# Kernel tuning notes

Measured on AMD Instinct MI355X. Metric: run time of the kernel, lower is better.

## Reference

```python
import jax, jax.numpy as jnp
import numpy as np

H = 16          # num_attention_heads
D = 1024        # hidden_size
HD = D // H     # attention_head_size = 64


def setup_inputs() -> dict:
    key = jax.random.key(0)
    ks = jax.random.split(key, 9)
    s = 1.0 / np.sqrt(D)
    return {
        "hidden_states": jax.random.normal(ks[0], (4, 1024, D), jnp.float32),
        "encoder_hidden_states": jax.random.normal(ks[1], (4, 1024, D), jnp.float32),
        "attention_mask": jnp.zeros((4, 1, 1, 2048), jnp.float32),
        "Wq": jax.random.normal(ks[2], (D, D), jnp.float32) * s,
        "bq": jnp.zeros((D,), jnp.float32),
        "Wk": jax.random.normal(ks[3], (D, D), jnp.float32) * s,
        "bk": jnp.zeros((D,), jnp.float32),
        "Wv": jax.random.normal(ks[4], (D, D), jnp.float32) * s,
        "bv": jnp.zeros((D,), jnp.float32),
    }


def _split_heads(x):
    # [B, S, D] -> [B, H, S, HD]
    B, S, _ = x.shape
    return x.reshape(B, S, H, HD).transpose(0, 2, 1, 3)


def reference(hidden_states, encoder_hidden_states, attention_mask, Wq, bq, Wk, bk, Wv, bv):
    # KV over concat(encoder, decoder); Q over decoder hidden states only.
    all_hidden = jnp.concatenate([encoder_hidden_states, hidden_states], axis=1)  # [B, Skv, D]
    q = _split_heads(hidden_states @ Wq + bq)        # [B, H, Sq, HD]
    k = _split_heads(all_hidden @ Wk + bk)           # [B, H, Skv, HD]
    v = _split_heads(all_hidden @ Wv + bv)           # [B, H, Skv, HD]

    scores = jnp.einsum("bhqd,bhkd->bhqk", q, k) / np.sqrt(HD).astype(np.float32)
    scores = scores + attention_mask                 # additive mask, broadcast
    probs = jax.nn.softmax(scores, axis=-1)          # dropout p=0 (eval)
    ctx = jnp.einsum("bhqk,bhkd->bhqd", probs, v)    # [B, H, Sq, HD]
    B, _, Sq, _ = ctx.shape
    return ctx.transpose(0, 2, 1, 3).reshape(B, Sq, D)
```

## Files before the change

### kernel.cpp

```cpp
#include <hip/hip_runtime.h>


typedef _Float16 f16;
typedef __attribute__((ext_vector_type(4))) _Float16 half4;
typedef __attribute__((ext_vector_type(8))) _Float16 half8;
typedef __attribute__((ext_vector_type(4))) float floatx4;
typedef __attribute__((ext_vector_type(16))) float floatx16;
typedef __attribute__((ext_vector_type(4))) unsigned int uint4v;

#define GLOAD16(gp, lp)                                                        \
    __builtin_amdgcn_global_load_lds(                                          \
        (const __attribute__((address_space(1))) void*)(gp),                   \
        (__attribute__((address_space(3))) void*)(lp), 16, 0, 0)

__global__ void wt_kernel(const float* __restrict__ Wq, const float* __restrict__ Wk,
                          const float* __restrict__ Wv, f16* __restrict__ Wtq,
                          f16* __restrict__ Wtk, f16* __restrict__ Wtv) {
    __shared__ float tile[32][33];
    const float* W = (blockIdx.z == 0) ? Wq : (blockIdx.z == 1) ? Wk : Wv;
    f16* Wt = (blockIdx.z == 0) ? Wtq : (blockIdx.z == 1) ? Wtk : Wtv;
    int k0 = blockIdx.y * 32, n0 = blockIdx.x * 32;
    int tx = threadIdx.x, ty = threadIdx.y;
    #pragma unroll
    for (int i = 0; i < 32; i += 8)
        tile[ty + i][tx] = W[(k0 + ty + i) * 1024 + n0 + tx];
    __syncthreads();
    #pragma unroll
    for (int i = 0; i < 32; i += 8)
        Wt[(n0 + ty + i) * 1024 + k0 + tx] = (f16)tile[tx][ty + i];
}

__global__ void cvt_kernel(const float* __restrict__ hid, const float* __restrict__ enc,
                           f16* __restrict__ Aall) {
    int t = blockIdx.x * 256 + threadIdx.x;
    int rowg = t >> 7, col = (t & 127) * 8;
    int b = rowg >> 11, r = rowg & 2047;
    const float* src = (r < 1024 ? enc + ((size_t)b * 1024 + r) * 1024
                                 : hid + ((size_t)b * 1024 + (r - 1024)) * 1024) + col;
    float4 v0 = *(const float4*)src, v1 = *(const float4*)(src + 4);
    half8 o;
    o[0] = (f16)v0.x; o[1] = (f16)v0.y; o[2] = (f16)v0.z; o[3] = (f16)v0.w;
    o[4] = (f16)v1.x; o[5] = (f16)v1.y; o[6] = (f16)v1.z; o[7] = (f16)v1.w;
    *(half8*)(Aall + (size_t)rowg * 1024 + col) = o;
}

__launch_bounds__(256)
__global__ void qkv_gemm(const f16* __restrict__ Aall,
                         const f16* __restrict__ Wtq, const f16* __restrict__ Wtk,
                         const f16* __restrict__ Wtv,
                         const float* __restrict__ bq, const float* __restrict__ bk,
                         const float* __restrict__ bv,
                         f16* __restrict__ Qw, f16* __restrict__ Kw, f16* __restrict__ Vtw) {
    int mode = blockIdx.z;
    if (mode == 0 && blockIdx.x >= 32) return;
    __shared__ f16 As[2][128 * 32];
    __shared__ f16 Bs[2][128 * 32];

    const f16* Wt = (mode == 0) ? Wtq : (mode == 1) ? Wtk : Wtv;
    const float* bias = (mode == 0) ? bq : (mode == 1) ? bk : bv;
    f16* out = (mode == 0) ? Qw : (mode == 1) ? Kw : Vtw;

    int tid = threadIdx.x;
    int m0 = blockIdx.x * 128, n0 = blockIdx.y * 128;
    int wid = tid >> 6, lane = tid & 63;
    int wm = (wid >> 1) * 64, wn = (wid & 1) * 64;
    int lr = lane & 15, lg = lane >> 4;

    floatx4 acc[4][4];
    #pragma unroll
    for (int i = 0; i < 4; i++)
        #pragma unroll
        for (int j = 0; j < 4; j++) acc[i][j] = (floatx4)(0.f);

    int trow = tid >> 2, tcol = (tid & 3) * 8;
    const f16 *a0g, *a1g;
    {
        int mA0 = m0 + trow, mA1 = mA0 + 64;
        if (mode == 0) {
            int b0 = mA0 >> 10, b1 = mA1 >> 10;
            a0g = Aall + ((size_t)(b0 * 2048 + 1024 + (mA0 & 1023))) * 1024 + tcol;
            a1g = Aall + ((size_t)(b1 * 2048 + 1024 + (mA1 & 1023))) * 1024 + tcol;
        } else {
            a0g = Aall + (size_t)mA0 * 1024 + tcol;
            a1g = Aall + (size_t)mA1 * 1024 + tcol;
        }
    }
    const f16* b0g = Wt + (size_t)(n0 + trow) * 1024 + tcol;
    const f16* b1g = Wt + (size_t)(n0 + trow + 64) * 1024 + tcol;

    GLOAD16(a0g, &As[0][tid * 8]);
    GLOAD16(a1g, &As[0][tid * 8 + 2048]);
    GLOAD16(b0g, &Bs[0][tid * 8]);
    GLOAD16(b1g, &Bs[0][tid * 8 + 2048]);
    __syncthreads();

    int cur = 0;
    for (int k0 = 0; k0 < 1024; k0 += 32) {
        if (k0 < 992) {
            int nx = cur ^ 1;
            GLOAD16(a0g + k0 + 32, &As[nx][tid * 8]);
            GLOAD16(a1g + k0 + 32, &As[nx][tid * 8 + 2048]);
            GLOAD16(b0g + k0 + 32, &Bs[nx][tid * 8]);
            GLOAD16(b1g + k0 + 32, &Bs[nx][tid * 8 + 2048]);
        }
        half8 a[4], bf[4];
        #pragma unroll
        for (int i = 0; i < 4; i++)
            a[i] = *(const half8*)&As[cur][(wm + i * 16 + lr) * 32 + lg * 8];
        #pragma unroll
        for (int j = 0; j < 4; j++)
            bf[j] = *(const half8*)&Bs[cur][(wn + j * 16 + lr) * 32 + lg * 8];
        __builtin_amdgcn_s_setprio(1);
        #pragma unroll
        for (int i = 0; i < 4; i++)
            #pragma unroll
            for (int j = 0; j < 4; j++)
                acc[i][j] = __builtin_amdgcn_mfma_f32_16x16x32_f16(a[i], bf[j], acc[i][j], 0, 0, 0);
        __builtin_amdgcn_s_setprio(0);
        __syncthreads();
        cur ^= 1;
    }

    if (mode == 2) {
        #pragma unroll
        for (int i = 0; i < 4; i++) {
            int mbase = m0 + wm + i * 16 + lg * 4;
            int b = mbase >> 11, s = mbase & 2047;
            #pragma unroll
            for (int j = 0; j < 4; j++) {
                int n = n0 + wn + j * 16 + lr;
                int h = n >> 6, d = n & 63;
                float bv = bias[n];
                half4 w;
                #pragma unroll
                for (int r = 0; r < 4; r++) w[r] = (f16)(acc[i][j][r] + bv);
                *(half4*)(out + ((size_t)((b * 16 + h) * 64 + d)) * 2048 + s) = w;
            }
        }
    } else {
        int Sout = (mode == 0) ? 1024 : 2048;
        #pragma unroll
        for (int i = 0; i < 4; i++) {
            int mbase = m0 + wm + i * 16 + lg * 4;
            #pragma unroll
            for (int j = 0; j < 4; j++) {
                int n = n0 + wn + j * 16 + lr;
                int h = n >> 6, d = n & 63;
                float bv = bias[n];
                #pragma unroll
                for (int r = 0; r < 4; r++) {
                    int m = mbase + r;
                    int b = (mode == 0) ? (m >> 10) : (m >> 11);
                    int s = (mode == 0) ? (m & 1023) : (m & 2047);
                    out[((size_t)(b * 16 + h) * Sout + s) * 64 + d] = (f16)(acc[i][j][r] + bv);
                }
            }
        }
    }
}

__device__ inline half8 pack_swap(float s0, float s1, float s2, float s3,
                                  float s4, float s5, float s6, float s7) {
    unsigned a0 = __builtin_bit_cast(unsigned, __builtin_amdgcn_cvt_pkrtz(s0, s1));
    unsigned b0 = __builtin_bit_cast(unsigned, __builtin_amdgcn_cvt_pkrtz(s4, s5));
    unsigned a1 = __builtin_bit_cast(unsigned, __builtin_amdgcn_cvt_pkrtz(s2, s3));
    unsigned b1 = __builtin_bit_cast(unsigned, __builtin_amdgcn_cvt_pkrtz(s6, s7));
    asm("v_permlane32_swap_b32 %0, %1" : "+v"(a0), "+v"(b0));
    asm("v_permlane32_swap_b32 %0, %1" : "+v"(a1), "+v"(b1));
    uint4v w = {a0, a1, b0, b1};
    return __builtin_bit_cast(half8, w);
}

__device__ inline half8 pack_noswap(float s0, float s1, float s2, float s3,
                                    float s4, float s5, float s6, float s7) {
    unsigned w0 = __builtin_bit_cast(unsigned, __builtin_amdgcn_cvt_pkrtz(s0, s1));
    unsigned w1 = __builtin_bit_cast(unsigned, __builtin_amdgcn_cvt_pkrtz(s2, s3));
    unsigned w2 = __builtin_bit_cast(unsigned, __builtin_amdgcn_cvt_pkrtz(s4, s5));
    unsigned w3 = __builtin_bit_cast(unsigned, __builtin_amdgcn_cvt_pkrtz(s6, s7));
    uint4v w = {w0, w1, w2, w3};
    return __builtin_bit_cast(half8, w);
}

__launch_bounds__(256)
__global__ void attn_kernel(const f16* __restrict__ Q, const f16* __restrict__ K,
                            const f16* __restrict__ Vt, const float* __restrict__ mask,
                            float* __restrict__ out) {
    __shared__ f16 Kt[2][64 * 72];
    __shared__ f16 Vtt[2][64 * 72];
    __shared__ float maskLds[2048];

    const float LOG2E = 1.4426950408889634f;
    int tid = threadIdx.x;
    int wid = tid >> 6, lane = tid & 63;
    int l31 = lane & 31, l5 = lane >> 5;

    int bid = blockIdx.x + 8 * blockIdx.y;
    int xcd = bid & 7, w = bid >> 3;
    int bh = xcd * 8 + (w >> 3);
    int xblk = w & 7;
    int b = bh >> 4;
    int q = xblk * 128 + wid * 32 + l31;

    half8 pa, pcode;
    #pragma unroll
    for (int j = 0; j < 8; j++) { pa[j] = (f16)0; pcode[j] = (f16)(8 * l5 + j); }
    if (l31 < 16 && (l31 >> 3) == l5) pa[l31 & 7] = (f16)1;
    floatx16 pd = __builtin_amdgcn_mfma_f32_32x32x16_f16(pa, pcode, (floatx16)0.f, 0, 0, 0);
    float r4 = __shfl(pd[0], 32);
    bool twoblk = (r4 > 6.0f);

    const float* maskp = mask + b * 2048;
    for (int i = tid; i < 512; i += 256) {
        float4 mv = ((const float4*)maskp)[i];
        mv.x *= LOG2E; mv.y *= LOG2E; mv.z *= LOG2E; mv.w *= LOG2E;
        ((float4*)maskLds)[i] = mv;
    }

    const f16* qrow = Q + ((size_t)bh * 1024 + q) * 64;
    half8 qf[4];
    if (!twoblk) {
        #pragma unroll
        for (int ks = 0; ks < 4; ks++)
            qf[ks] = *(const half8*)(qrow + ks * 16 + l5 * 8);
    } else {
        #pragma unroll
        for (int ks = 0; ks < 4; ks++) {
            half4 lo = *(const half4*)(qrow + ks * 16 + 4 * l5);
            half4 hi = *(const half4*)(qrow + ks * 16 + 8 + 4 * l5);
            qf[ks][0] = lo[0]; qf[ks][1] = lo[1]; qf[ks][2] = lo[2]; qf[ks][3] = lo[3];
            qf[ks][4] = hi[0]; qf[ks][5] = hi[1]; qf[ks][6] = hi[2]; qf[ks][7] = hi[3];
        }
    }
    const f16 qs = (f16)(0.125f * 1.4426950408889634f);
    #pragma unroll
    for (int ks = 0; ks < 4; ks++)
        #pragma unroll
        for (int x = 0; x < 8; x++) qf[ks][x] *= qs;

    floatx16 o0 = (floatx16)0.f, o1 = (floatx16)0.f;
    float m_run = 8.0f, l_run = 0.f;

    int sr = tid >> 2, sc = (tid & 3) * 16;
    const f16* Ksrc = K + ((size_t)bh * 2048 + sr) * 64 + sc;
    const f16* Vsrc = Vt + ((size_t)(bh * 64 + sr)) * 2048 + sc;

    half8 rk0 = *(const half8*)(Ksrc);
    half8 rk1 = *(const half8*)(Ksrc + 8);
    half8 rv0 = *(const half8*)(Vsrc);
    half8 rv1 = *(const half8*)(Vsrc + 8);
    *(half8*)&Kt[0][sr * 72 + sc]      = rk0;
    *(half8*)&Kt[0][sr * 72 + sc + 8]  = rk1;
    *(half8*)&Vtt[0][sr * 72 + sc]     = rv0;
    *(half8*)&Vtt[0][sr * 72 + sc + 8] = rv1;
    rk0 = *(const half8*)(Ksrc + (size_t)64 * 64);
    rk1 = *(const half8*)(Ksrc + (size_t)64 * 64 + 8);
    rv0 = *(const half8*)(Vsrc + 64);
    rv1 = *(const half8*)(Vsrc + 64 + 8);
    __syncthreads();

    int cur = 0;
    for (int kv0 = 0; kv0 < 2048; kv0 += 64) {
        if (kv0 < 2048 - 64) {
            int nx = cur ^ 1;
            *(half8*)&Kt[nx][sr * 72 + sc]      = rk0;
            *(half8*)&Kt[nx][sr * 72 + sc + 8]  = rk1;
            *(half8*)&Vtt[nx][sr * 72 + sc]     = rv0;
            *(half8*)&Vtt[nx][sr * 72 + sc + 8] = rv1;
            if (kv0 < 2048 - 128) {
                rk0 = *(const half8*)(Ksrc + (size_t)(kv0 + 128) * 64);
                rk1 = *(const half8*)(Ksrc + (size_t)(kv0 + 128) * 64 + 8);
                rv0 = *(const half8*)(Vsrc + kv0 + 128);
                rv1 = *(const half8*)(Vsrc + kv0 + 128 + 8);
            }
        }

        floatx16 sf0, sf1;
        #pragma unroll
        for (int g = 0; g < 4; g++) {
            float4 mk0 = *(const float4*)&maskLds[kv0 + 8 * g + 4 * l5];
            float4 mk1 = *(const float4*)&maskLds[kv0 + 32 + 8 * g + 4 * l5];
            #pragma unroll
            for (int i = 0; i < 4; i++) {
                sf0[4 * g + i] = ((const float*)&mk0)[i];
                sf1[4 * g + i] = ((const float*)&mk1)[i];
            }
        }

        __builtin_amdgcn_s_setprio(1);
        #pragma unroll
        for (int ks = 0; ks < 4; ks++) {
            half8 k0 = *(const half8*)&Kt[cur][l31 * 72 + ks * 16 + l5 * 8];
            half8 k1 = *(const half8*)&Kt[cur][(32 + l31) * 72 + ks * 16 + l5 * 8];
            sf0 = __builtin_amdgcn_mfma_f32_32x32x16_f16(k0, qf[ks], sf0, 0, 0, 0);
            sf1 = __builtin_amdgcn_mfma_f32_32x32x16_f16(k1, qf[ks], sf1, 0, 0, 0);
        }
        __builtin_amdgcn_s_setprio(0);

        float pmax = -1e30f;
        #pragma unroll
        for (int r = 0; r < 16; r++)
            pmax = fmaxf(pmax, fmaxf(sf0[r], sf1[r]));

        if (!__all(pmax - m_run <= 8.0f)) {
            float rmax = fmaxf(pmax, __shfl_xor(pmax, 32));
            float mnew = fmaxf(m_run, rmax);
            float alpha = exp2f(m_run - mnew);
            l_run *= alpha;
            #pragma unroll
            for (int r = 0; r < 16; r++) { o0[r] *= alpha; o1[r] *= alpha; }
            m_run = mnew;
        }

        float ls = 0.f;
        #pragma unroll
        for (int r = 0; r < 16; r++) {
            float p0 = exp2f(sf0[r] - m_run);
            float p1 = exp2f(sf1[r] - m_run);
            sf0[r] = p0; sf1[r] = p1;
            ls += p0 + p1;
        }
        ls += __shfl_xor(ls, 32);
        l_run += ls;

        half8 pb[4];
        if (!twoblk) {
            pb[0] = pack_swap(sf0[0], sf0[1], sf0[2], sf0[3], sf0[4], sf0[5], sf0[6], sf0[7]);
            pb[1] = pack_swap(sf0[8], sf0[9], sf0[10], sf0[11], sf0[12], sf0[13], sf0[14], sf0[15]);
            pb[2] = pack_swap(sf1[0], sf1[1], sf1[2], sf1[3], sf1[4], sf1[5], sf1[6], sf1[7]);
            pb[3] = pack_swap(sf1[8], sf1[9], sf1[10], sf1[11], sf1[12], sf1[13], sf1[14], sf1[15]);
        } else {
            pb[0] = pack_noswap(sf0[0], sf0[1], sf0[2], sf0[3], sf0[4], sf0[5], sf0[6], sf0[7]);
            pb[1] = pack_noswap(sf0[8], sf0[9], sf0[10], sf0[11], sf0[12], sf0[13], sf0[14], sf0[15]);
            pb[2] = pack_noswap(sf1[0], sf1[1], sf1[2], sf1[3], sf1[4], sf1[5], sf1[6], sf1[7]);
            pb[3] = pack_noswap(sf1[8], sf1[9], sf1[10], sf1[11], sf1[12], sf1[13], sf1[14], sf1[15]);
        }

        __builtin_amdgcn_s_setprio(1);
        #pragma unroll
        for (int kb = 0; kb < 4; kb++) {
            half8 v0 = *(const half8*)&Vtt[cur][l31 * 72 + kb * 16 + l5 * 8];
            half8 v1 = *(const half8*)&Vtt[cur][(32 + l31) * 72 + kb * 16 + l5 * 8];
            o0 = __builtin_amdgcn_mfma_f32_32x32x16_f16(v0, pb[kb], o0, 0, 0, 0);
            o1 = __builtin_amdgcn_mfma_f32_32x32x16_f16(v1, pb[kb], o1, 0, 0, 0);
        }
        __builtin_amdgcn_s_setprio(0);

        __syncthreads();
        cur ^= 1;
    }

    int h = bh & 15;
    float inv = 1.f / l_run;
    float* orow = out + ((size_t)(b * 1024 + q)) * 1024 + h * 64;
    #pragma unroll
    for (int g = 0; g < 4; g++) {
        float4 r0 = {o0[4 * g] * inv, o0[4 * g + 1] * inv, o0[4 * g + 2] * inv, o0[4 * g + 3] * inv};
        float4 r1 = {o1[4 * g] * inv, o1[4 * g + 1] * inv, o1[4 * g + 2] * inv, o1[4 * g + 3] * inv};
        *(float4*)&orow[8 * g + 4 * l5]      = r0;
        *(float4*)&orow[32 + 8 * g + 4 * l5] = r1;
    }
}

extern "C" void kernel_launch(void* const* d_in, const int* in_sizes, int n_in,
                              void* d_out, int out_size, void* d_ws, size_t ws_size,
                              hipStream_t stream) {
    const float* hid  = (const float*)d_in[0];
    const float* enc  = (const float*)d_in[1];
    const float* mask = (const float*)d_in[2];
    const float* Wq   = (const float*)d_in[3];
    const float* bq   = (const float*)d_in[4];
    const float* Wk   = (const float*)d_in[5];
    const float* bk   = (const float*)d_in[6];
    const float* Wv   = (const float*)d_in[7];
    const float* bv   = (const float*)d_in[8];
    float* out = (float*)d_out;

    char* ws = (char*)d_ws;
    f16* Wtq  = (f16*)(ws + ((size_t)0 << 20));
    f16* Wtk  = (f16*)(ws + ((size_t)2 << 20));
    f16* Wtv  = (f16*)(ws + ((size_t)4 << 20));
    f16* Aall = (f16*)(ws + ((size_t)6 << 20));
    f16* Qw   = (f16*)(ws + ((size_t)22 << 20));
    f16* Kw   = (f16*)(ws + ((size_t)30 << 20));
    f16* Vtw  = (f16*)(ws + ((size_t)46 << 20));

    wt_kernel<<<dim3(32, 32, 3), dim3(32, 8), 0, stream>>>(Wq, Wk, Wv, Wtq, Wtk, Wtv);
    cvt_kernel<<<4096, 256, 0, stream>>>(hid, enc, Aall);

    qkv_gemm<<<dim3(64, 8, 3), 256, 0, stream>>>(Aall, Wtq, Wtk, Wtv, bq, bk, bv, Qw, Kw, Vtw);

    attn_kernel<<<dim3(8, 64), 256, 0, stream>>>(Qw, Kw, Vtw, mask, out);
}
```

Measured before the change: 155.1 us.

## Merge prep kernels, compute softmax row sums via MFMA, tree-reduce row max

Merges the weight-transpose and activation-convert kernels into one launch, removing a kernel boundary. In the attention loop, the softmax denominator is now accumulated by an extra MFMA that multiplies a ones-vector by the probability tile, replacing the scalar sum and cross-lane shuffle. The row max is computed with a tree of three-input maxes to shorten the dependency chain. The extra MFMA per kv step adds matrix-core work and an accumulator register block, which may raise register pressure.

```diff
diff --git a/kernel.cpp b/kernel.cpp
--- a/kernel.cpp
+++ b/kernel.cpp
@@ -13,35 +13,38 @@
         (const __attribute__((address_space(1))) void*)(gp),                   \
         (__attribute__((address_space(3))) void*)(lp), 16, 0, 0)
 
-__global__ void wt_kernel(const float* __restrict__ Wq, const float* __restrict__ Wk,
-                          const float* __restrict__ Wv, f16* __restrict__ Wtq,
-                          f16* __restrict__ Wtk, f16* __restrict__ Wtv) {
-    __shared__ float tile[32][33];
-    const float* W = (blockIdx.z == 0) ? Wq : (blockIdx.z == 1) ? Wk : Wv;
-    f16* Wt = (blockIdx.z == 0) ? Wtq : (blockIdx.z == 1) ? Wtk : Wtv;
-    int k0 = blockIdx.y * 32, n0 = blockIdx.x * 32;
-    int tx = threadIdx.x, ty = threadIdx.y;
-    #pragma unroll
-    for (int i = 0; i < 32; i += 8)
-        tile[ty + i][tx] = W[(k0 + ty + i) * 1024 + n0 + tx];
-    __syncthreads();
-    #pragma unroll
-    for (int i = 0; i < 32; i += 8)
-        Wt[(n0 + ty + i) * 1024 + k0 + tx] = (f16)tile[tx][ty + i];
-}
-
-__global__ void cvt_kernel(const float* __restrict__ hid, const float* __restrict__ enc,
-                           f16* __restrict__ Aall) {
-    int t = blockIdx.x * 256 + threadIdx.x;
-    int rowg = t >> 7, col = (t & 127) * 8;
-    int b = rowg >> 11, r = rowg & 2047;
-    const float* src = (r < 1024 ? enc + ((size_t)b * 1024 + r) * 1024
-                                 : hid + ((size_t)b * 1024 + (r - 1024)) * 1024) + col;
-    float4 v0 = *(const float4*)src, v1 = *(const float4*)(src + 4);
-    half8 o;
-    o[0] = (f16)v0.x; o[1] = (f16)v0.y; o[2] = (f16)v0.z; o[3] = (f16)v0.w;
-    o[4] = (f16)v1.x; o[5] = (f16)v1.y; o[6] = (f16)v1.z; o[7] = (f16)v1.w;
-    *(half8*)(Aall + (size_t)rowg * 1024 + col) = o;
+__global__ void prep_kernel(const float* __restrict__ hid, const float* __restrict__ enc,
+                            const float* __restrict__ Wq, const float* __restrict__ Wk,
+                            const float* __restrict__ Wv, f16* __restrict__ Wtq,
+                            f16* __restrict__ Wtk, f16* __restrict__ Wtv,
+                            f16* __restrict__ Aall) {
+    int bid = blockIdx.x, tid = threadIdx.x;
+    if (bid < 3072) {
+        __shared__ float tile[32][33];
+        int z = bid >> 10, xy = bid & 1023;
+        const float* W = (z == 0) ? Wq : (z == 1) ? Wk : Wv;
+        f16* Wt = (z == 0) ? Wtq : (z == 1) ? Wtk : Wtv;
+        int n0 = (xy & 31) * 32, k0 = (xy >> 5) * 32;
+        int tx = tid & 31, ty = tid >> 5;
+        #pragma unroll
+        for (int i = 0; i < 32; i += 8)
+            tile[ty + i][tx] = W[(k0 + ty + i) * 1024 + n0 + tx];
+        __syncthreads();
+        #pragma unroll
+        for (int i = 0; i < 32; i += 8)
+            Wt[(n0 + ty + i) * 1024 + k0 + tx] = (f16)tile[tx][ty + i];
+    } else {
+        int t = (bid - 3072) * 256 + tid;
+        int rowg = t >> 7, col = (t & 127) * 8;
+        int b = rowg >> 11, r = rowg & 2047;
+        const float* src = (r < 1024 ? enc + ((size_t)b * 1024 + r) * 1024
+                                     : hid + ((size_t)b * 1024 + (r - 1024)) * 1024) + col;
+        float4 v0 = *(const float4*)src, v1 = *(const float4*)(src + 4);
+        half8 o;
+        o[0] = (f16)v0.x; o[1] = (f16)v0.y; o[2] = (f16)v0.z; o[3] = (f16)v0.w;
+        o[4] = (f16)v1.x; o[5] = (f16)v1.y; o[6] = (f16)v1.z; o[7] = (f16)v1.w;
+        *(half8*)(Aall + (size_t)rowg * 1024 + col) = o;
+    }
 }
 
 __launch_bounds__(256)
@@ -181,6 +184,8 @@
     return __builtin_bit_cast(half8, w);
 }
 
+#define SS(r) ((r) < 16 ? sf0[(r)] : sf1[(r) - 16])
+
 __launch_bounds__(256)
 __global__ void attn_kernel(const f16* __restrict__ Q, const f16* __restrict__ K,
                             const f16* __restrict__ Vt, const float* __restrict__ mask,
@@ -237,8 +242,12 @@
         #pragma unroll
         for (int x = 0; x < 8; x++) qf[ks][x] *= qs;
 
-    floatx16 o0 = (floatx16)0.f, o1 = (floatx16)0.f;
-    float m_run = 8.0f, l_run = 0.f;
+    half8 aones;
+    #pragma unroll
+    for (int j = 0; j < 8; j++) aones[j] = (l31 == 0) ? (f16)1 : (f16)0;
+
+    floatx16 o0 = (floatx16)0.f, o1 = (floatx16)0.f, o2 = (floatx16)0.f;
+    float m_run = 8.0f;
 
     int sr = tid >> 2, sc = (tid & 3) * 16;
     const f16* Ksrc = K + ((size_t)bh * 2048 + sr) * 64 + sc;
@@ -296,31 +305,31 @@
         }
         __builtin_amdgcn_s_setprio(0);
 
-        float pmax = -1e30f;
-        #pragma unroll
-        for (int r = 0; r < 16; r++)
-            pmax = fmaxf(pmax, fmaxf(sf0[r], sf1[r]));
+        float mx[11];
+        #pragma unroll
+        for (int t = 0; t < 10; t++)
+            mx[t] = fmaxf(fmaxf(SS(3 * t), SS(3 * t + 1)), SS(3 * t + 2));
+        mx[10] = fmaxf(SS(30), SS(31));
+        float pmax = fmaxf(fmaxf(mx[0], mx[1]), mx[2]);
+        float p2 = fmaxf(fmaxf(mx[3], mx[4]), mx[5]);
+        float p3 = fmaxf(fmaxf(mx[6], mx[7]), mx[8]);
+        float p4 = fmaxf(fmaxf(mx[9], mx[10]), pmax);
+        pmax = fmaxf(fmaxf(p2, p3), p4);
 
         if (!__all(pmax - m_run <= 8.0f)) {
             float rmax = fmaxf(pmax, __shfl_xor(pmax, 32));
             float mnew = fmaxf(m_run, rmax);
             float alpha = exp2f(m_run - mnew);
-            l_run *= alpha;
             #pragma unroll
-            for (int r = 0; r < 16; r++) { o0[r] *= alpha; o1[r] *= alpha; }
+            for (int r = 0; r < 16; r++) { o0[r] *= alpha; o1[r] *= alpha; o2[r] *= alpha; }
             m_run = mnew;
         }
 
-        float ls = 0.f;
         #pragma unroll
         for (int r = 0; r < 16; r++) {
-            float p0 = exp2f(sf0[r] - m_run);
-            float p1 = exp2f(sf1[r] - m_run);
-            sf0[r] = p0; sf1[r] = p1;
-            ls += p0 + p1;
-        }
-        ls += __shfl_xor(ls, 32);
-        l_run += ls;
+            sf0[r] = exp2f(sf0[r] - m_run);
+            sf1[r] = exp2f(sf1[r] - m_run);
+        }
 
         half8 pb[4];
         if (!twoblk) {
@@ -342,6 +351,7 @@
             half8 v1 = *(const half8*)&Vtt[cur][(32 + l31) * 72 + kb * 16 + l5 * 8];
             o0 = __builtin_amdgcn_mfma_f32_32x32x16_f16(v0, pb[kb], o0, 0, 0, 0);
             o1 = __builtin_amdgcn_mfma_f32_32x32x16_f16(v1, pb[kb], o1, 0, 0, 0);
+            o2 = __builtin_amdgcn_mfma_f32_32x32x16_f16(aones, pb[kb], o2, 0, 0, 0);
         }
         __builtin_amdgcn_s_setprio(0);
 
@@ -349,8 +359,9 @@
         cur ^= 1;
     }
 
+    float l_all = __shfl(o2[0], l31);
     int h = bh & 15;
-    float inv = 1.f / l_run;
+    float inv = 1.f / l_all;
     float* orow = out + ((size_t)(b * 1024 + q)) * 1024 + h * 64;
     #pragma unroll
     for (int g = 0; g < 4; g++) {
@@ -384,8 +395,7 @@
     f16* Kw   = (f16*)(ws + ((size_t)30 << 20));
     f16* Vtw  = (f16*)(ws + ((size_t)46 << 20));
 
-    wt_kernel<<<dim3(32, 32, 3), dim3(32, 8), 0, stream>>>(Wq, Wk, Wv, Wtq, Wtk, Wtv);
-    cvt_kernel<<<4096, 256, 0, stream>>>(hid, enc, Aall);
+    prep_kernel<<<7168, 256, 0, stream>>>(hid, enc, Wq, Wk, Wv, Wtq, Wtk, Wtv, Aall);
 
     qkv_gemm<<<dim3(64, 8, 3), 256, 0, stream>>>(Aall, Wtq, Wtk, Wtv, bq, bk, bv, Qw, Kw, Vtw);
 
```

After: 150.7 us. -2.8%, faster.
